# Kernel tuning notes

Hardware: AMD Instinct MI355X
Metric: run time of the kernel (lower is better)

Reference implementation:

```python
import math
import jax, jax.numpy as jnp
import numpy as np

B, W_LEN, C = 4, 2048, 768
H = 3  # fixed number of heads in the module
K = C // H  # head dim


def setup_inputs() -> dict:
    key = jax.random.key(0)
    k1, k2, k3 = jax.random.split(key, 3)
    in_sequence_bwc = jax.random.normal(k1, (B, W_LEN, C), dtype=jnp.float32)
    # torch nn.Linear weights: [out_features, in_features], scaled for stability
    W_qkv = jax.random.normal(k2, (3 * C, C), dtype=jnp.float32) * (1.0 / math.sqrt(C))
    W_proj = jax.random.normal(k3, (C, C), dtype=jnp.float32) * (1.0 / math.sqrt(C))
    return {"in_sequence_bwc": in_sequence_bwc, "W_qkv": W_qkv, "W_proj": W_proj}


def reference(in_sequence_bwc, W_qkv, W_proj):
    batch, words, coords = in_sequence_bwc.shape
    head_dim = coords // H
    # qkv projection: x @ W^T  -> [b, w, 3c]
    all_bwd = jnp.einsum("bwc,dc->bwd", in_sequence_bwc, W_qkv)
    q_bwc, k_bwc, v_bwc = jnp.split(all_bwd, 3, axis=-1)
    # [b, h, w, k]
    q = q_bwc.reshape(batch, words, H, head_dim).transpose(0, 2, 1, 3)
    k = k_bwc.reshape(batch, words, H, head_dim).transpose(0, 2, 1, 3)
    v = v_bwc.reshape(batch, words, H, head_dim).transpose(0, 2, 1, 3)
    # scaled scores with causal mask -> softmax -> @V
    scores = jnp.einsum("bhqk,bhmk->bhqm", q, k) / math.sqrt(head_dim)
    causal = jnp.tril(jnp.ones((words, words), dtype=bool))
    scores = jnp.where(causal[None, None], scores, -jnp.inf)
    probs = jax.nn.softmax(scores, axis=-1)
    out = jnp.einsum("bhqm,bhmk->bhqk", probs, v)
    out_bwc = out.transpose(0, 2, 1, 3).reshape(batch, words, coords)
    return jnp.einsum("bwc,dc->bwd", out_bwc, W_proj)
```

## Files before the change

### kernel.cpp

```cpp
#include <hip/hip_runtime.h>

using v8h = __attribute__((ext_vector_type(8))) _Float16;
using v4f = __attribute__((ext_vector_type(4))) float;
using v4u = __attribute__((ext_vector_type(4))) unsigned short;
using v8u = __attribute__((ext_vector_type(8))) unsigned short;

__device__ __forceinline__ unsigned short f2h(float x) {
  _Float16 h = (_Float16)x;
  return __builtin_bit_cast(unsigned short, h);
}
__device__ __forceinline__ float h2f(unsigned short u) {
  return (float)__builtin_bit_cast(_Float16, u);
}

__device__ __forceinline__ void gl_lds16(const unsigned short* g, unsigned short* l) {
  __builtin_amdgcn_global_load_lds(
      (const __attribute__((address_space(1))) unsigned int*)g,
      (__attribute__((address_space(3))) unsigned int*)l, 16, 0, 0);
}

__global__ void cvt3_kernel(const float* __restrict__ X,
                            const float* __restrict__ Wq,
                            const float* __restrict__ Wp,
                            unsigned short* __restrict__ Xb,
                            unsigned short* __restrict__ Wqb,
                            unsigned short* __restrict__ Wpb) {
  const int blk = (int)blockIdx.x;
  const float* src;
  unsigned short* dst;
  int i;
  if (blk < 3072)      { src = X;  dst = Xb;  i = blk * 256 + threadIdx.x; }
  else if (blk < 3936) { src = Wq; dst = Wqb; i = (blk - 3072) * 256 + threadIdx.x; }
  else                 { src = Wp; dst = Wpb; i = (blk - 3936) * 256 + threadIdx.x; }
  const float* p = src + (size_t)i * 8;
  float4 a = *(const float4*)p;
  float4 b = *(const float4*)(p + 4);
  v8u o = {f2h(a.x), f2h(a.y), f2h(a.z), f2h(a.w),
           f2h(b.x), f2h(b.y), f2h(b.z), f2h(b.w)};
  *(v8u*)(dst + (size_t)i * 8) = o;
}

__global__ __launch_bounds__(512, 2)
void qkv8_kernel(const unsigned short* __restrict__ A,
                 const unsigned short* __restrict__ Bw,
                 unsigned short* __restrict__ QK) {
  __shared__ unsigned short sm[65536];
  const int t    = (int)threadIdx.x;
  const int ln   = t & 63;
  const int wv   = t >> 6;
  const int quad = ln >> 4;
  const int L    = ln & 15;
  const int wm   = wv >> 2;
  const int wn   = wv & 3;
  const long m0  = (long)blockIdx.y * 256;
  const long n0  = (long)blockIdx.x * 256;

  const int srow = t >> 3;
  const int scol = ((t & 7) ^ (srow & 7)) * 8;
  const unsigned short* Ath = A + (m0 + srow) * 768 + scol;
  const unsigned short* Bth = Bw + (n0 + srow) * 768 + scol;
  unsigned short* lth = &sm[t * 8];

  const int l7   = L & 7;
  const int sl0  = ((0 + quad) ^ l7) * 8;
  const int sl1  = ((4 + quad) ^ l7) * 8;
  const int arow = (wm * 128 + L) * 64;
  const int brow = (wn * 64 + L) * 64;

  v4f acc[8][4];
#pragma unroll
  for (int i = 0; i < 8; i++)
#pragma unroll
    for (int j = 0; j < 4; j++) acc[i][j] = (v4f){0.f, 0.f, 0.f, 0.f};

  auto stA = [&](int tile, int h) {
    if (tile >= 12) return;
    const unsigned short* g = Ath + (h * 128) * 768 + tile * 64;
    unsigned short* l = lth + (tile & 1) * 32768 + h * 8192;
    gl_lds16(g, l);
    gl_lds16(g + 64 * 768, l + 4096);
  };
  auto stB = [&](int tile, int h) {
    if (tile >= 12) return;
    const unsigned short* g = Bth + (h * 128) * 768 + tile * 64;
    unsigned short* l = lth + (tile & 1) * 32768 + 16384 + h * 8192;
    gl_lds16(g, l);
    gl_lds16(g + 64 * 768, l + 4096);
  };

  stB(0, 0); stB(0, 1); stA(0, 0); stA(0, 1);
  stB(1, 0); stB(1, 1); stA(1, 0);
  asm volatile("s_waitcnt vmcnt(6)" ::: "memory");
  __builtin_amdgcn_s_barrier();
  __builtin_amdgcn_sched_barrier(0);

#pragma unroll 2
  for (int kt = 0; kt < 12; ++kt) {
    const unsigned short* sA = &sm[(kt & 1) * 32768];
    const unsigned short* sB = sA + 16384;
    v8h af[4][2], b0[2][2], b1[2][2];

#pragma unroll
    for (int i = 0; i < 4; i++) {
      af[i][0] = *(const v8h*)&sA[arow + i * 1024 + sl0];
      af[i][1] = *(const v8h*)&sA[arow + i * 1024 + sl1];
    }
#pragma unroll
    for (int j = 0; j < 2; j++) {
      b0[j][0] = *(const v8h*)&sB[brow + j * 1024 + sl0];
      b0[j][1] = *(const v8h*)&sB[brow + j * 1024 + sl1];
    }
    stA(kt + 1, 1);
    __builtin_amdgcn_s_barrier();
    asm volatile("s_waitcnt lgkmcnt(0)" ::: "memory");
    __builtin_amdgcn_sched_barrier(0);
    __builtin_amdgcn_s_setprio(1);
#pragma unroll
    for (int i = 0; i < 4; i++)
#pragma unroll
      for (int j = 0; j < 2; j++) {
        acc[i][j] = __builtin_amdgcn_mfma_f32_16x16x32_f16(af[i][0], b0[j][0], acc[i][j], 0, 0, 0);
        acc[i][j] = __builtin_amdgcn_mfma_f32_16x16x32_f16(af[i][1], b0[j][1], acc[i][j], 0, 0, 0);
      }
    __builtin_amdgcn_s_setprio(0);
    __builtin_amdgcn_s_barrier();
    __builtin_amdgcn_sched_barrier(0);

#pragma unroll
    for (int j = 0; j < 2; j++) {
      b1[j][0] = *(const v8h*)&sB[brow + 2048 + j * 1024 + sl0];
      b1[j][1] = *(const v8h*)&sB[brow + 2048 + j * 1024 + sl1];
    }
    __builtin_amdgcn_s_barrier();
    asm volatile("s_waitcnt lgkmcnt(0)" ::: "memory");
    __builtin_amdgcn_sched_barrier(0);
    __builtin_amdgcn_s_setprio(1);
#pragma unroll
    for (int i = 0; i < 4; i++)
#pragma unroll
      for (int j = 0; j < 2; j++) {
        acc[i][2 + j] = __builtin_amdgcn_mfma_f32_16x16x32_f16(af[i][0], b1[j][0], acc[i][2 + j], 0, 0, 0);
        acc[i][2 + j] = __builtin_amdgcn_mfma_f32_16x16x32_f16(af[i][1], b1[j][1], acc[i][2 + j], 0, 0, 0);
      }
    __builtin_amdgcn_s_setprio(0);
    __builtin_amdgcn_s_barrier();
    __builtin_amdgcn_sched_barrier(0);

#pragma unroll
    for (int i = 0; i < 4; i++) {
      af[i][0] = *(const v8h*)&sA[arow + 4096 + i * 1024 + sl0];
      af[i][1] = *(const v8h*)&sA[arow + 4096 + i * 1024 + sl1];
    }
    stB(kt + 2, 0);
    __builtin_amdgcn_s_barrier();
    asm volatile("s_waitcnt lgkmcnt(0)" ::: "memory");
    __builtin_amdgcn_sched_barrier(0);
    __builtin_amdgcn_s_setprio(1);
#pragma unroll
    for (int i = 0; i < 4; i++)
#pragma unroll
      for (int j = 0; j < 2; j++) {
        acc[4 + i][2 + j] = __builtin_amdgcn_mfma_f32_16x16x32_f16(af[i][0], b1[j][0], acc[4 + i][2 + j], 0, 0, 0);
        acc[4 + i][2 + j] = __builtin_amdgcn_mfma_f32_16x16x32_f16(af[i][1], b1[j][1], acc[4 + i][2 + j], 0, 0, 0);
      }
    __builtin_amdgcn_s_setprio(0);
    __builtin_amdgcn_s_barrier();
    __builtin_amdgcn_sched_barrier(0);

    stB(kt + 2, 1);
    stA(kt + 2, 0);
    __builtin_amdgcn_s_barrier();
    __builtin_amdgcn_sched_barrier(0);
    __builtin_amdgcn_s_setprio(1);
#pragma unroll
    for (int i = 0; i < 4; i++)
#pragma unroll
      for (int j = 0; j < 2; j++) {
        acc[4 + i][j] = __builtin_amdgcn_mfma_f32_16x16x32_f16(af[i][0], b0[j][0], acc[4 + i][j], 0, 0, 0);
        acc[4 + i][j] = __builtin_amdgcn_mfma_f32_16x16x32_f16(af[i][1], b0[j][1], acc[4 + i][j], 0, 0, 0);
      }
    __builtin_amdgcn_s_setprio(0);
    if (kt + 2 < 12)      { asm volatile("s_waitcnt vmcnt(6)" ::: "memory"); }
    else if (kt + 1 < 12) { asm volatile("s_waitcnt vmcnt(0)" ::: "memory"); }
    __builtin_amdgcn_s_barrier();
    __builtin_amdgcn_sched_barrier(0);
  }

#pragma unroll
  for (int mi = 0; mi < 8; mi++) {
    const long row = m0 + wm * 128 + (mi >> 2) * 64 + (mi & 3) * 16 + quad * 4;
#pragma unroll
    for (int nj = 0; nj < 4; nj++) {
      const long col = n0 + wn * 64 + nj * 16 + L;
#pragma unroll
      for (int r = 0; r < 4; r++)
        QK[(row + r) * 1536 + col] = f2h(acc[mi][nj][r]);
    }
  }
}

__global__ __launch_bounds__(512, 2)
void scv8_kernel(const unsigned short* __restrict__ QK,
                 const unsigned short* __restrict__ Xb,
                 const unsigned short* __restrict__ Wq,
                 unsigned short* __restrict__ Sc,
                 unsigned short* __restrict__ VT) {
  __shared__ unsigned short sm[65536];
  const int t    = (int)threadIdx.x;
  const int ln   = t & 63;
  const int wv   = t >> 6;
  const int quad = ln >> 4;
  const int L    = ln & 15;
  const int wm   = wv >> 2;
  const int wn   = wv & 3;

  const int x = (int)blockIdx.x;
  const bool isV = (x < 96);
  int NT, Ihi = 0, Jhi = 0, bh = 0, mt = 0, nt = 0;
  const unsigned short* Abase;
  const unsigned short* Bbase;
  long astr, bstr;

  if (isV) {
    mt = x & 31;
    nt = x >> 5;
    Abase = Xb + (long)mt * 256 * 768;
    Bbase = Wq + (long)(1536 + nt * 256) * 768;
    astr = 768; bstr = 768; NT = 12;
  } else {
    int s = x - 96;
    bh = s / 36;
    int slot = s % 36;
    while (slot >= Ihi + 1) { slot -= Ihi + 1; Ihi++; }
    Jhi = slot;
    const int b = bh / 3, h = bh % 3;
    Abase = QK + ((long)b * 2048 + Ihi * 256) * 1536 + h * 256;
    Bbase = QK + ((long)b * 2048 + Jhi * 256) * 1536 + 768 + h * 256;
    astr = 1536; bstr = 1536; NT = 4;
  }

  const int srow = t >> 3;
  const int scol = ((t & 7) ^ (srow & 7)) * 8;
  const unsigned short* Ath = Abase + (long)srow * astr + scol;
  const unsigned short* Bth = Bbase + (long)srow * bstr + scol;
  unsigned short* lth = &sm[t * 8];

  const int l7   = L & 7;
  const int sl0  = ((0 + quad) ^ l7) * 8;
  const int sl1  = ((4 + quad) ^ l7) * 8;
  const int arow = (wm * 128 + L) * 64;
  const int brow = (wn * 64 + L) * 64;

  v4f acc[8][4];
#pragma unroll
  for (int i = 0; i < 8; i++)
#pragma unroll
    for (int j = 0; j < 4; j++) acc[i][j] = (v4f){0.f, 0.f, 0.f, 0.f};

  auto stA = [&](int tile, int h) {
    if (tile >= NT) return;
    const unsigned short* g = Ath + (long)(h * 128) * astr + tile * 64;
    unsigned short* l = lth + (tile & 1) * 32768 + h * 8192;
    gl_lds16(g, l);
    gl_lds16(g + 64 * astr, l + 4096);
  };
  auto stB = [&](int tile, int h) {
    if (tile >= NT) return;
    const unsigned short* g = Bth + (long)(h * 128) * bstr + tile * 64;
    unsigned short* l = lth + (tile & 1) * 32768 + 16384 + h * 8192;
    gl_lds16(g, l);
    gl_lds16(g + 64 * bstr, l + 4096);
  };

  stB(0, 0); stB(0, 1); stA(0, 0); stA(0, 1);
  stB(1, 0); stB(1, 1); stA(1, 0);
  asm volatile("s_waitcnt vmcnt(6)" ::: "memory");
  __builtin_amdgcn_s_barrier();
  __builtin_amdgcn_sched_barrier(0);

#pragma unroll 2
  for (int kt = 0; kt < NT; ++kt) {
    const unsigned short* sA = &sm[(kt & 1) * 32768];
    const unsigned short* sB = sA + 16384;
    v8h af[4][2], b0[2][2], b1[2][2];

#pragma unroll
    for (int i = 0; i < 4; i++) {
      af[i][0] = *(const v8h*)&sA[arow + i * 1024 + sl0];
      af[i][1] = *(const v8h*)&sA[arow + i * 1024 + sl1];
    }
#pragma unroll
    for (int j = 0; j < 2; j++) {
      b0[j][0] = *(const v8h*)&sB[brow + j * 1024 + sl0];
      b0[j][1] = *(const v8h*)&sB[brow + j * 1024 + sl1];
    }
    stA(kt + 1, 1);
    __builtin_amdgcn_s_barrier();
    asm volatile("s_waitcnt lgkmcnt(0)" ::: "memory");
    __builtin_amdgcn_sched_barrier(0);
    __builtin_amdgcn_s_setprio(1);
#pragma unroll
    for (int i = 0; i < 4; i++)
#pragma unroll
      for (int j = 0; j < 2; j++) {
        acc[i][j] = __builtin_amdgcn_mfma_f32_16x16x32_f16(af[i][0], b0[j][0], acc[i][j], 0, 0, 0);
        acc[i][j] = __builtin_amdgcn_mfma_f32_16x16x32_f16(af[i][1], b0[j][1], acc[i][j], 0, 0, 0);
      }
    __builtin_amdgcn_s_setprio(0);
    __builtin_amdgcn_s_barrier();
    __builtin_amdgcn_sched_barrier(0);

#pragma unroll
    for (int j = 0; j < 2; j++) {
      b1[j][0] = *(const v8h*)&sB[brow + 2048 + j * 1024 + sl0];
      b1[j][1] = *(const v8h*)&sB[brow + 2048 + j * 1024 + sl1];
    }
    __builtin_amdgcn_s_barrier();
    asm volatile("s_waitcnt lgkmcnt(0)" ::: "memory");
    __builtin_amdgcn_sched_barrier(0);
    __builtin_amdgcn_s_setprio(1);
#pragma unroll
    for (int i = 0; i < 4; i++)
#pragma unroll
      for (int j = 0; j < 2; j++) {
        acc[i][2 + j] = __builtin_amdgcn_mfma_f32_16x16x32_f16(af[i][0], b1[j][0], acc[i][2 + j], 0, 0, 0);
        acc[i][2 + j] = __builtin_amdgcn_mfma_f32_16x16x32_f16(af[i][1], b1[j][1], acc[i][2 + j], 0, 0, 0);
      }
    __builtin_amdgcn_s_setprio(0);
    __builtin_amdgcn_s_barrier();
    __builtin_amdgcn_sched_barrier(0);

#pragma unroll
    for (int i = 0; i < 4; i++) {
      af[i][0] = *(const v8h*)&sA[arow + 4096 + i * 1024 + sl0];
      af[i][1] = *(const v8h*)&sA[arow + 4096 + i * 1024 + sl1];
    }
    stB(kt + 2, 0);
    __builtin_amdgcn_s_barrier();
    asm volatile("s_waitcnt lgkmcnt(0)" ::: "memory");
    __builtin_amdgcn_sched_barrier(0);
    __builtin_amdgcn_s_setprio(1);
#pragma unroll
    for (int i = 0; i < 4; i++)
#pragma unroll
      for (int j = 0; j < 2; j++) {
        acc[4 + i][2 + j] = __builtin_amdgcn_mfma_f32_16x16x32_f16(af[i][0], b1[j][0], acc[4 + i][2 + j], 0, 0, 0);
        acc[4 + i][2 + j] = __builtin_amdgcn_mfma_f32_16x16x32_f16(af[i][1], b1[j][1], acc[4 + i][2 + j], 0, 0, 0);
      }
    __builtin_amdgcn_s_setprio(0);
    __builtin_amdgcn_s_barrier();
    __builtin_amdgcn_sched_barrier(0);

    stB(kt + 2, 1);
    stA(kt + 2, 0);
    __builtin_amdgcn_s_barrier();
    __builtin_amdgcn_sched_barrier(0);
    __builtin_amdgcn_s_setprio(1);
#pragma unroll
    for (int i = 0; i < 4; i++)
#pragma unroll
      for (int j = 0; j < 2; j++) {
        acc[4 + i][j] = __builtin_amdgcn_mfma_f32_16x16x32_f16(af[i][0], b0[j][0], acc[4 + i][j], 0, 0, 0);
        acc[4 + i][j] = __builtin_amdgcn_mfma_f32_16x16x32_f16(af[i][1], b0[j][1], acc[4 + i][j], 0, 0, 0);
      }
    __builtin_amdgcn_s_setprio(0);
    if (kt + 2 < NT)      { asm volatile("s_waitcnt vmcnt(6)" ::: "memory"); }
    else if (kt + 1 < NT) { asm volatile("s_waitcnt vmcnt(0)" ::: "memory"); }
    __builtin_amdgcn_s_barrier();
    __builtin_amdgcn_sched_barrier(0);
  }

  if (isV) {
#pragma unroll
    for (int mi = 0; mi < 8; mi++) {
      const long token = (long)mt * 256 + wm * 128 + (mi >> 2) * 64 + (mi & 3) * 16 + quad * 4;
      const int b  = (int)(token >> 11);
      const int tk = (int)(token & 2047);
#pragma unroll
      for (int nj = 0; nj < 4; nj++) {
        const int colp = nt * 256 + wn * 64 + nj * 16 + L;
        const int h    = colp >> 8;
        const int d    = colp & 255;
        v4u val = {f2h(acc[mi][nj][0]), f2h(acc[mi][nj][1]),
                   f2h(acc[mi][nj][2]), f2h(acc[mi][nj][3])};
        *(v4u*)(&VT[((long)(b * 3 + h) * 256 + d) * 2048 + tk]) = val;
      }
    }
  } else {
    const int di = wm;
    const int dj = wn >> 1;
    const int i128 = 2 * Ihi + di;
    const int j128 = 2 * Jhi + dj;
    if (j128 <= i128) {
      unsigned short* Sb = Sc + ((long)bh * 136 + (long)i128 * (i128 + 1) / 2 + j128) * 16384;
#pragma unroll
      for (int mi = 0; mi < 8; mi++) {
        const int subrow = (mi >> 2) * 64 + (mi & 3) * 16 + quad * 4;
#pragma unroll
        for (int nj = 0; nj < 4; nj++) {
          const int subcol = (wn & 1) * 64 + nj * 16 + L;
#pragma unroll
          for (int r = 0; r < 4; r++)
            Sb[(subrow + r) * 128 + subcol] = f2h(acc[mi][nj][r]);
        }
      }
    }
  }
}

__global__ __launch_bounds__(256, 2)
void gemm_proj_kernel(const unsigned short* __restrict__ A,
                      const unsigned short* __restrict__ Bw,
                      float* __restrict__ C) {
  __shared__ unsigned short As[4096];
  __shared__ unsigned short Bs[4096];

  const int t    = threadIdx.x;
  const int ln   = t & 63;
  const int wv   = t >> 6;
  const int quad = ln >> 4;
  const int L    = ln & 15;
  const int wm   = (wv >> 1) * 64;
  const int wn   = (wv & 1) * 64;
  const long m0  = (long)blockIdx.y * 128;
  const long n0  = (long)blockIdx.x * 128;

  v4f acc[4][4];
#pragma unroll
  for (int i = 0; i < 4; i++)
#pragma unroll
    for (int j = 0; j < 4; j++) acc[i][j] = (v4f){0.f, 0.f, 0.f, 0.f};

  const int ar = t >> 2;
  const int ac = (t & 3) * 8;
  const unsigned short* Ag = A + (m0 + ar) * 768 + ac;
  const unsigned short* Bg = Bw + (n0 + ar) * 768 + ac;
  unsigned short* la = &As[t * 8];
  unsigned short* lb = &Bs[t * 8];
  const long rowskip = 64L * 768;

  for (int k0 = 0; k0 < 768; k0 += 32) {
    gl_lds16(Ag + k0, la);
    gl_lds16(Ag + rowskip + k0, la + 2048);
    gl_lds16(Bg + k0, lb);
    gl_lds16(Bg + rowskip + k0, lb + 2048);
    __syncthreads();

    v8h af[4], bfr[4];
#pragma unroll
    for (int i = 0; i < 4; i++)
      af[i] = *(const v8h*)(&As[(wm + i * 16 + L) * 32 + quad * 8]);
#pragma unroll
    for (int j = 0; j < 4; j++)
      bfr[j] = *(const v8h*)(&Bs[(wn + j * 16 + L) * 32 + quad * 8]);
#pragma unroll
    for (int i = 0; i < 4; i++)
#pragma unroll
      for (int j = 0; j < 4; j++)
        acc[i][j] = __builtin_amdgcn_mfma_f32_16x16x32_f16(af[i], bfr[j], acc[i][j], 0, 0, 0);
    __syncthreads();
  }

#pragma unroll
  for (int i = 0; i < 4; i++)
#pragma unroll
    for (int j = 0; j < 4; j++)
#pragma unroll
      for (int r = 0; r < 4; r++) {
        long row = m0 + wm + i * 16 + quad * 4 + r;
        long col = n0 + wn + j * 16 + L;
        C[row * 768 + col] = acc[i][j][r];
      }
}

__global__ __launch_bounds__(256, 4)
void softmax_kernel(unsigned short* __restrict__ Sc) {
  const int tt   = threadIdx.x;
  const int wv   = tt >> 6;
  const int lane = tt & 63;
  const int bh   = (int)blockIdx.y;

  const int r = 2047 - ((int)blockIdx.x * 4 + wv);
  const int i = r >> 7;
  const int rowloc = r & 127;
  const long base = ((long)bh * 136 + (long)i * (i + 1) / 2) * 16384 + rowloc * 128;
  const int Lrow = (i + 1) * 128;
  const int nch = (i + 4) >> 2;

  float xs[4][8];
  float mx = -1e30f;
  for (int k = 0; k < nch; k++) {
    int c0 = k * 512 + lane * 8;
    if (c0 < Lrow) {
      int j = c0 >> 7;
      v8u v = *(const v8u*)(Sc + base + (long)j * 16384 + (c0 & 127));
#pragma unroll
      for (int e = 0; e < 8; e++) {
        float f = (c0 + e <= r) ? h2f(v[e]) * 0.0625f : -1e30f;
        xs[k][e] = f;
        mx = fmaxf(mx, f);
      }
    } else {
#pragma unroll
      for (int e = 0; e < 8; e++) xs[k][e] = -1e30f;
    }
  }
#pragma unroll
  for (int d = 1; d < 64; d <<= 1) mx = fmaxf(mx, __shfl_xor(mx, d));

  float sum = 0.f;
  for (int k = 0; k < nch; k++)
#pragma unroll
    for (int e = 0; e < 8; e++) {
      float ex = __expf(xs[k][e] - mx);
      xs[k][e] = ex;
      sum += ex;
    }
#pragma unroll
  for (int d = 1; d < 64; d <<= 1) sum += __shfl_xor(sum, d);
  const float inv = 1.0f / sum;

  for (int k = 0; k < nch; k++) {
    int c0 = k * 512 + lane * 8;
    if (c0 < Lrow) {
      int j = c0 >> 7;
      v8u o;
#pragma unroll
      for (int e = 0; e < 8; e++) o[e] = f2h(xs[k][e] * inv);
      *(v8u*)(Sc + base + (long)j * 16384 + (c0 & 127)) = o;
    }
  }
}

__global__ __launch_bounds__(256, 2)
void gemm_pv_kernel(const unsigned short* __restrict__ Sc,
                    const unsigned short* __restrict__ VT,
                    unsigned short* __restrict__ Pp) {
  __shared__ unsigned short As[4096];
  __shared__ unsigned short Bs[4096];

  const int t    = threadIdx.x;
  const int ln   = t & 63;
  const int wv   = t >> 6;
  const int quad = ln >> 4;
  const int L    = ln & 15;
  const int wm   = (wv >> 1) * 64;
  const int wn   = (wv & 1) * 64;

  const int ix  = (int)blockIdx.x;
  const int i   = 15 - (ix >> 2);
  const int nh  = (ix >> 1) & 1;
  const int par = ix & 1;
  const int bh  = (int)blockIdx.y;

  v4f acc[4][4];
#pragma unroll
  for (int ii = 0; ii < 4; ii++)
#pragma unroll
    for (int jj = 0; jj < 4; jj++) acc[ii][jj] = (v4f){0.f, 0.f, 0.f, 0.f};

  const int ar = t >> 2;
  const int ac = (t & 3) * 8;
  const unsigned short* Abase =
      Sc + ((long)bh * 136 + (long)i * (i + 1) / 2) * 16384 + ar * 128 + ac;
  const unsigned short* Bg =
      VT + ((long)bh * 256 + nh * 128 + ar) * 2048 + ac;
  unsigned short* la = &As[t * 8];
  unsigned short* lb = &Bs[t * 8];

  for (int j = par; j <= i; j += 2) {
    const unsigned short* Aj = Abase + (long)j * 16384;
    const unsigned short* Bj = Bg + j * 128;
#pragma unroll
    for (int k0 = 0; k0 < 128; k0 += 32) {
      gl_lds16(Aj + k0, la);
      gl_lds16(Aj + 64 * 128 + k0, la + 2048);
      gl_lds16(Bj + k0, lb);
      gl_lds16(Bj + 64 * 2048 + k0, lb + 2048);
      __syncthreads();

      v8h af[4], bfr[4];
#pragma unroll
      for (int ii = 0; ii < 4; ii++)
        af[ii] = *(const v8h*)(&As[(wm + ii * 16 + L) * 32 + quad * 8]);
#pragma unroll
      for (int jj = 0; jj < 4; jj++)
        bfr[jj] = *(const v8h*)(&Bs[(wn + jj * 16 + L) * 32 + quad * 8]);
#pragma unroll
      for (int ii = 0; ii < 4; ii++)
#pragma unroll
        for (int jj = 0; jj < 4; jj++)
          acc[ii][jj] = __builtin_amdgcn_mfma_f32_16x16x32_f16(af[ii], bfr[jj], acc[ii][jj], 0, 0, 0);
      __syncthreads();
    }
  }

  unsigned short* Pb = Pp + ((((long)bh * 16 + i) * 2 + nh) * 2 + par) * 16384;
#pragma unroll
  for (int ii = 0; ii < 4; ii++)
#pragma unroll
    for (int jj = 0; jj < 4; jj++)
#pragma unroll
      for (int r = 0; r < 4; r++) {
        int row = wm + ii * 16 + quad * 4 + r;
        int col = wn + jj * 16 + L;
        Pb[row * 128 + col] = f2h(acc[ii][jj][r]);
      }
}

__global__ __launch_bounds__(256, 4)
void pv_combine_kernel(const unsigned short* __restrict__ Pp,
                       unsigned short* __restrict__ AO) {
  const int i  = (int)blockIdx.x >> 1;
  const int nh = (int)blockIdx.x & 1;
  const int bh = (int)blockIdx.y;
  const int b  = bh / 3, h = bh % 3;

  const int tid = threadIdx.x;
  const int row = tid >> 1;
  const int cs  = (tid & 1) * 64;

  const unsigned short* P0 = Pp + ((((long)bh * 16 + i) * 2 + nh) * 2 + 0) * 16384 + row * 128 + cs;
  const unsigned short* P1 = P0 + 16384;
  unsigned short* Or = AO + ((long)b * 2048 + i * 128 + row) * 768 + h * 256 + nh * 128 + cs;
#pragma unroll
  for (int q = 0; q < 8; q++) {
    v8u a = *(const v8u*)(P0 + q * 8);
    v8u c = *(const v8u*)(P1 + q * 8);
    v8u o;
#pragma unroll
    for (int e = 0; e < 8; e++) o[e] = f2h(h2f(a[e]) + h2f(c[e]));
    *(v8u*)(Or + q * 8) = o;
  }
}

extern "C" void kernel_launch(void* const* d_in, const int* in_sizes, int n_in,
                              void* d_out, int out_size, void* d_ws, size_t ws_size,
                              hipStream_t stream) {
  const float* X     = (const float*)d_in[0];
  const float* Wqkv  = (const float*)d_in[1];
  const float* Wproj = (const float*)d_in[2];
  float* out = (float*)d_out;

  const size_t SZ_QK = (size_t)8192 * 1536 * 2;
  const size_t SZ_VT = (size_t)3072 * 2048 * 2;
  const size_t SZ_SC = (size_t)12 * 136 * 16384 * 2;
  const size_t SZ_AO = (size_t)8192 * 768 * 2;
  const size_t SZ_WQ = (size_t)2304 * 768 * 2;

  char* ws = (char*)d_ws;
  unsigned short* QKb = (unsigned short*)ws;
  unsigned short* Ppb = QKb;
  unsigned short* VTb = (unsigned short*)(ws + SZ_QK);
  unsigned short* Scb = (unsigned short*)(ws + SZ_QK + SZ_VT);
  unsigned short* AOb = (unsigned short*)(ws + SZ_QK + SZ_VT + SZ_SC);
  unsigned short* Xb  = AOb;
  unsigned short* Wqb = (unsigned short*)(ws + SZ_QK + SZ_VT + SZ_SC + SZ_AO);
  unsigned short* Wpb = (unsigned short*)(ws + SZ_QK + SZ_VT + SZ_SC + SZ_AO + SZ_WQ);

  dim3 blk(256, 1, 1);
  cvt3_kernel<<<dim3(4224, 1, 1), blk, 0, stream>>>(X, Wqkv, Wproj, Xb, Wqb, Wpb);
  qkv8_kernel<<<dim3(6, 32, 1), dim3(512, 1, 1), 0, stream>>>(Xb, Wqb, QKb);
  scv8_kernel<<<dim3(528, 1, 1), dim3(512, 1, 1), 0, stream>>>(QKb, Xb, Wqb, Scb, VTb);
  softmax_kernel<<<dim3(512, 12, 1), blk, 0, stream>>>(Scb);
  gemm_pv_kernel<<<dim3(64, 12, 1), blk, 0, stream>>>(Scb, VTb, Ppb);
  pv_combine_kernel<<<dim3(32, 12, 1), blk, 0, stream>>>(Ppb, AOb);
  gemm_proj_kernel<<<dim3(6, 64, 1), blk, 0, stream>>>(AOb, Wpb, out);
}
```

Before: 243.6 us.

## Fuse softmax, PV GEMM and combine into one online-softmax kernel

Replaces the separate softmax pass, the split-K PV GEMM and the partial-sum combine kernel with one kernel. It runs an online (flash-style) softmax over the stored fp16 score tiles and multiplies by V with MFMA, double-buffering V tiles in swizzled LDS and prefetching score fragments into registers. Blocks pair query tile i with tile 15-i to balance the causal work. This drops the softmax read-modify-write of the score matrix and the partial-product round trip. The cost is a much smaller grid (192 blocks of 512 threads), so parallelism is lower, and the loop relies on manual waitcnt and barrier scheduling.

Result: faster. 223.6 us (-8.2%).

```diff
diff --git a/kernel.cpp b/kernel.cpp
--- a/kernel.cpp
+++ b/kernel.cpp
@@ -408,6 +408,186 @@
   }
 }
 
+__global__ __launch_bounds__(512, 1)
+void pvf_kernel(const unsigned short* __restrict__ Sc,
+                const unsigned short* __restrict__ VT,
+                unsigned short* __restrict__ AO) {
+  __shared__ unsigned short sm[36864];
+  __shared__ float fbuf[128];
+
+  const int t    = (int)threadIdx.x;
+  const int ln   = t & 63;
+  const int wv   = t >> 6;
+  const int quad = ln >> 4;
+  const int L    = ln & 15;
+
+  const int p  = (int)blockIdx.x >> 1;
+  const int nh = (int)blockIdx.x & 1;
+  const int bh = (int)blockIdx.y;
+  const int b  = bh / 3, h = bh % 3;
+
+  const unsigned short* VTb = VT + ((long)(bh * 256 + nh * 128)) * 2048;
+  const int rloc = wv * 16 + L;
+
+  auto stageV = [&](int jj, unsigned short* base) {
+#pragma unroll
+    for (int pp = 0; pp < 4; pp++) {
+      const int sidx = pp * 512 + t;
+      const int d    = sidx >> 4;
+      const int ph   = sidx & 15;
+      gl_lds16(VTb + (long)d * 2048 + jj * 128 + ((ph ^ (d & 7)) * 8),
+               base + sidx * 8);
+    }
+  };
+
+  for (int sel = 0; sel < 2; ++sel) {
+    const int i = sel ? (15 - p) : p;
+    const long Sbase = ((long)bh * 136 + (long)i * (i + 1) / 2) * 16384;
+
+    v4f acc[8];
+#pragma unroll
+    for (int n = 0; n < 8; n++) acc[n] = (v4f){0.f, 0.f, 0.f, 0.f};
+    float m_run = -1e30f, l_run = 0.f;
+
+    v8u s_cur[4], s_nxt[4];
+    {
+      const unsigned short* Sp = Sc + Sbase + (long)rloc * 128;
+#pragma unroll
+      for (int ks = 0; ks < 4; ks++)
+        s_cur[ks] = *(const v8u*)(Sp + ks * 32 + quad * 8);
+      __builtin_amdgcn_sched_barrier(0);
+      stageV(0, &sm[0]);
+      __builtin_amdgcn_sched_barrier(0);
+    }
+
+    for (int j = 0; j <= i; ++j) {
+      const int jn = (j < i) ? (j + 1) : i;
+      const bool clamped = (j == i);
+      {
+        const unsigned short* Sp = Sc + Sbase + (long)jn * 16384 + (long)rloc * 128;
+#pragma unroll
+        for (int ks = 0; ks < 4; ks++)
+          s_nxt[ks] = *(const v8u*)(Sp + ks * 32 + quad * 8);
+      }
+      __builtin_amdgcn_sched_barrier(0);
+      if (clamped) {
+#pragma unroll
+        for (int pp = 0; pp < 4; pp++) {
+          const int sidx = pp * 512 + t;
+          const int d    = sidx >> 4;
+          const int ph   = sidx & 15;
+          gl_lds16(VTb + (long)d * 2048 + jn * 128 + ((ph ^ (d & 7)) * 8),
+                   &sm[32768 + t * 8]);
+        }
+      } else {
+        stageV(jn, &sm[(jn & 1) * 16384]);
+      }
+      __builtin_amdgcn_sched_barrier(0);
+
+      float pv[4][8];
+      float mx = -1e30f;
+      if (j == i) {
+#pragma unroll
+        for (int ks = 0; ks < 4; ks++)
+#pragma unroll
+          for (int e = 0; e < 8; e++) {
+            const bool valid = (ks * 32 + quad * 8 + e) <= rloc;
+            const float f = valid ? h2f(s_cur[ks][e]) * 0.0625f : -1e30f;
+            pv[ks][e] = f;
+            mx = fmaxf(mx, f);
+          }
+      } else {
+#pragma unroll
+        for (int ks = 0; ks < 4; ks++)
+#pragma unroll
+          for (int e = 0; e < 8; e++) {
+            const float f = h2f(s_cur[ks][e]) * 0.0625f;
+            pv[ks][e] = f;
+            mx = fmaxf(mx, f);
+          }
+      }
+      mx = fmaxf(mx, __shfl_xor(mx, 16));
+      mx = fmaxf(mx, __shfl_xor(mx, 32));
+      const float m_new = fmaxf(m_run, mx);
+      const float alpha = __expf(m_run - m_new);
+      m_run = m_new;
+
+      float sum = 0.f;
+      v8h pa[4];
+#pragma unroll
+      for (int ks = 0; ks < 4; ks++) {
+        v8h ph16;
+#pragma unroll
+        for (int e = 0; e < 8; e++) {
+          const float pe = __expf(pv[ks][e] - m_new);
+          sum += pe;
+          ph16[e] = (_Float16)pe;
+        }
+        pa[ks] = ph16;
+      }
+      sum += __shfl_xor(sum, 16);
+      sum += __shfl_xor(sum, 32);
+      l_run = l_run * alpha + sum;
+
+      if (quad == 0) fbuf[wv * 16 + L] = alpha;
+      asm volatile("s_waitcnt lgkmcnt(0)" ::: "memory");
+      __builtin_amdgcn_sched_barrier(0);
+      const float a0 = fbuf[wv * 16 + quad * 4 + 0];
+      const float a1 = fbuf[wv * 16 + quad * 4 + 1];
+      const float a2 = fbuf[wv * 16 + quad * 4 + 2];
+      const float a3 = fbuf[wv * 16 + quad * 4 + 3];
+#pragma unroll
+      for (int n = 0; n < 8; n++) {
+        acc[n][0] *= a0; acc[n][1] *= a1; acc[n][2] *= a2; acc[n][3] *= a3;
+      }
+
+      asm volatile("s_waitcnt vmcnt(8)" ::: "memory");
+      __builtin_amdgcn_s_barrier();
+      __builtin_amdgcn_sched_barrier(0);
+
+      const unsigned short* vb = &sm[(j & 1) * 16384];
+      const int dx = L & 7;
+#pragma unroll
+      for (int nfc = 0; nfc < 8; nfc++) {
+        const int dbase = (nfc * 16 + L) * 128;
+        v8h v0 = *(const v8h*)&vb[dbase + ((0 + quad) ^ dx) * 8];
+        v8h v1 = *(const v8h*)&vb[dbase + ((4 + quad) ^ dx) * 8];
+        v8h v2 = *(const v8h*)&vb[dbase + ((8 + quad) ^ dx) * 8];
+        v8h v3 = *(const v8h*)&vb[dbase + ((12 + quad) ^ dx) * 8];
+        acc[nfc] = __builtin_amdgcn_mfma_f32_16x16x32_f16(pa[0], v0, acc[nfc], 0, 0, 0);
+        acc[nfc] = __builtin_amdgcn_mfma_f32_16x16x32_f16(pa[1], v1, acc[nfc], 0, 0, 0);
+        acc[nfc] = __builtin_amdgcn_mfma_f32_16x16x32_f16(pa[2], v2, acc[nfc], 0, 0, 0);
+        acc[nfc] = __builtin_amdgcn_mfma_f32_16x16x32_f16(pa[3], v3, acc[nfc], 0, 0, 0);
+      }
+      __builtin_amdgcn_s_barrier();
+      __builtin_amdgcn_sched_barrier(0);
+
+#pragma unroll
+      for (int ks = 0; ks < 4; ks++) s_cur[ks] = s_nxt[ks];
+    }
+
+    const float inv = 1.0f / l_run;
+    if (quad == 0) fbuf[wv * 16 + L] = inv;
+    asm volatile("s_waitcnt lgkmcnt(0)" ::: "memory");
+    __builtin_amdgcn_sched_barrier(0);
+    const float i0 = fbuf[wv * 16 + quad * 4 + 0];
+    const float i1 = fbuf[wv * 16 + quad * 4 + 1];
+    const float i2 = fbuf[wv * 16 + quad * 4 + 2];
+    const float i3 = fbuf[wv * 16 + quad * 4 + 3];
+
+    unsigned short* Ob = AO + ((long)b * 2048 + (long)i * 128 + wv * 16 + quad * 4) * 768
+                            + h * 256 + nh * 128 + L;
+#pragma unroll
+    for (int n = 0; n < 8; n++) {
+      Ob[0 * 768 + n * 16] = f2h(acc[n][0] * i0);
+      Ob[1 * 768 + n * 16] = f2h(acc[n][1] * i1);
+      Ob[2 * 768 + n * 16] = f2h(acc[n][2] * i2);
+      Ob[3 * 768 + n * 16] = f2h(acc[n][3] * i3);
+    }
+    __builtin_amdgcn_s_barrier();
+  }
+}
+
 __global__ __launch_bounds__(256, 2)
 void gemm_proj_kernel(const unsigned short* __restrict__ A,
                       const unsigned short* __restrict__ Bw,
@@ -473,167 +653,6 @@
       }
 }
 
-__global__ __launch_bounds__(256, 4)
-void softmax_kernel(unsigned short* __restrict__ Sc) {
-  const int tt   = threadIdx.x;
-  const int wv   = tt >> 6;
-  const int lane = tt & 63;
-  const int bh   = (int)blockIdx.y;
-
-  const int r = 2047 - ((int)blockIdx.x * 4 + wv);
-  const int i = r >> 7;
-  const int rowloc = r & 127;
-  const long base = ((long)bh * 136 + (long)i * (i + 1) / 2) * 16384 + rowloc * 128;
-  const int Lrow = (i + 1) * 128;
-  const int nch = (i + 4) >> 2;
-
-  float xs[4][8];
-  float mx = -1e30f;
-  for (int k = 0; k < nch; k++) {
-    int c0 = k * 512 + lane * 8;
-    if (c0 < Lrow) {
-      int j = c0 >> 7;
-      v8u v = *(const v8u*)(Sc + base + (long)j * 16384 + (c0 & 127));
-#pragma unroll
-      for (int e = 0; e < 8; e++) {
-        float f = (c0 + e <= r) ? h2f(v[e]) * 0.0625f : -1e30f;
-        xs[k][e] = f;
-        mx = fmaxf(mx, f);
-      }
-    } else {
-#pragma unroll
-      for (int e = 0; e < 8; e++) xs[k][e] = -1e30f;
-    }
-  }
-#pragma unroll
-  for (int d = 1; d < 64; d <<= 1) mx = fmaxf(mx, __shfl_xor(mx, d));
-
-  float sum = 0.f;
-  for (int k = 0; k < nch; k++)
-#pragma unroll
-    for (int e = 0; e < 8; e++) {
-      float ex = __expf(xs[k][e] - mx);
-      xs[k][e] = ex;
-      sum += ex;
-    }
-#pragma unroll
-  for (int d = 1; d < 64; d <<= 1) sum += __shfl_xor(sum, d);
-  const float inv = 1.0f / sum;
-
-  for (int k = 0; k < nch; k++) {
-    int c0 = k * 512 + lane * 8;
-    if (c0 < Lrow) {
-      int j = c0 >> 7;
-      v8u o;
-#pragma unroll
-      for (int e = 0; e < 8; e++) o[e] = f2h(xs[k][e] * inv);
-      *(v8u*)(Sc + base + (long)j * 16384 + (c0 & 127)) = o;
-    }
-  }
-}
-
-__global__ __launch_bounds__(256, 2)
-void gemm_pv_kernel(const unsigned short* __restrict__ Sc,
-                    const unsigned short* __restrict__ VT,
-                    unsigned short* __restrict__ Pp) {
-  __shared__ unsigned short As[4096];
-  __shared__ unsigned short Bs[4096];
-
-  const int t    = threadIdx.x;
-  const int ln   = t & 63;
-  const int wv   = t >> 6;
-  const int quad = ln >> 4;
-  const int L    = ln & 15;
-  const int wm   = (wv >> 1) * 64;
-  const int wn   = (wv & 1) * 64;
-
-  const int ix  = (int)blockIdx.x;
-  const int i   = 15 - (ix >> 2);
-  const int nh  = (ix >> 1) & 1;
-  const int par = ix & 1;
-  const int bh  = (int)blockIdx.y;
-
-  v4f acc[4][4];
-#pragma unroll
-  for (int ii = 0; ii < 4; ii++)
-#pragma unroll
-    for (int jj = 0; jj < 4; jj++) acc[ii][jj] = (v4f){0.f, 0.f, 0.f, 0.f};
-
-  const int ar = t >> 2;
-  const int ac = (t & 3) * 8;
-  const unsigned short* Abase =
-      Sc + ((long)bh * 136 + (long)i * (i + 1) / 2) * 16384 + ar * 128 + ac;
-  const unsigned short* Bg =
-      VT + ((long)bh * 256 + nh * 128 + ar) * 2048 + ac;
-  unsigned short* la = &As[t * 8];
-  unsigned short* lb = &Bs[t * 8];
-
-  for (int j = par; j <= i; j += 2) {
-    const unsigned short* Aj = Abase + (long)j * 16384;
-    const unsigned short* Bj = Bg + j * 128;
-#pragma unroll
-    for (int k0 = 0; k0 < 128; k0 += 32) {
-      gl_lds16(Aj + k0, la);
-      gl_lds16(Aj + 64 * 128 + k0, la + 2048);
-      gl_lds16(Bj + k0, lb);
-      gl_lds16(Bj + 64 * 2048 + k0, lb + 2048);
-      __syncthreads();
-
-      v8h af[4], bfr[4];
-#pragma unroll
-      for (int ii = 0; ii < 4; ii++)
-        af[ii] = *(const v8h*)(&As[(wm + ii * 16 + L) * 32 + quad * 8]);
-#pragma unroll
-      for (int jj = 0; jj < 4; jj++)
-        bfr[jj] = *(const v8h*)(&Bs[(wn + jj * 16 + L) * 32 + quad * 8]);
-#pragma unroll
-      for (int ii = 0; ii < 4; ii++)
-#pragma unroll
-        for (int jj = 0; jj < 4; jj++)
-          acc[ii][jj] = __builtin_amdgcn_mfma_f32_16x16x32_f16(af[ii], bfr[jj], acc[ii][jj], 0, 0, 0);
-      __syncthreads();
-    }
-  }
-
-  unsigned short* Pb = Pp + ((((long)bh * 16 + i) * 2 + nh) * 2 + par) * 16384;
-#pragma unroll
-  for (int ii = 0; ii < 4; ii++)
-#pragma unroll
-    for (int jj = 0; jj < 4; jj++)
-#pragma unroll
-      for (int r = 0; r < 4; r++) {
-        int row = wm + ii * 16 + quad * 4 + r;
-        int col = wn + jj * 16 + L;
-        Pb[row * 128 + col] = f2h(acc[ii][jj][r]);
-      }
-}
-
-__global__ __launch_bounds__(256, 4)
-void pv_combine_kernel(const unsigned short* __restrict__ Pp,
-                       unsigned short* __restrict__ AO) {
-  const int i  = (int)blockIdx.x >> 1;
-  const int nh = (int)blockIdx.x & 1;
-  const int bh = (int)blockIdx.y;
-  const int b  = bh / 3, h = bh % 3;
-
-  const int tid = threadIdx.x;
-  const int row = tid >> 1;
-  const int cs  = (tid & 1) * 64;
-
-  const unsigned short* P0 = Pp + ((((long)bh * 16 + i) * 2 + nh) * 2 + 0) * 16384 + row * 128 + cs;
-  const unsigned short* P1 = P0 + 16384;
-  unsigned short* Or = AO + ((long)b * 2048 + i * 128 + row) * 768 + h * 256 + nh * 128 + cs;
-#pragma unroll
-  for (int q = 0; q < 8; q++) {
-    v8u a = *(const v8u*)(P0 + q * 8);
-    v8u c = *(const v8u*)(P1 + q * 8);
-    v8u o;
-#pragma unroll
-    for (int e = 0; e < 8; e++) o[e] = f2h(h2f(a[e]) + h2f(c[e]));
-    *(v8u*)(Or + q * 8) = o;
-  }
-}
-
 extern "C" void kernel_launch(void* const* d_in, const int* in_sizes, int n_in,
                               void* d_out, int out_size, void* d_ws, size_t ws_size,
                               hipStream_t stream) {
@@ -650,7 +669,6 @@
 
   char* ws = (char*)d_ws;
   unsigned short* QKb = (unsigned short*)ws;
-  unsigned short* Ppb = QKb;
   unsigned short* VTb = (unsigned short*)(ws + SZ_QK);
   unsigned short* Scb = (unsigned short*)(ws + SZ_QK + SZ_VT);
   unsigned short* AOb = (unsigned short*)(ws + SZ_QK + SZ_VT + SZ_SC);
@@ -662,8 +680,6 @@
   cvt3_kernel<<<dim3(4224, 1, 1), blk, 0, stream>>>(X, Wqkv, Wproj, Xb, Wqb, Wpb);
   qkv8_kernel<<<dim3(6, 32, 1), dim3(512, 1, 1), 0, stream>>>(Xb, Wqb, QKb);
   scv8_kernel<<<dim3(528, 1, 1), dim3(512, 1, 1), 0, stream>>>(QKb, Xb, Wqb, Scb, VTb);
-  softmax_kernel<<<dim3(512, 12, 1), blk, 0, stream>>>(Scb);
-  gemm_pv_kernel<<<dim3(64, 12, 1), blk, 0, stream>>>(Scb, VTb, Ppb);
-  pv_combine_kernel<<<dim3(32, 12, 1), blk, 0, stream>>>(Ppb, AOb);
+  pvf_kernel<<<dim3(16, 12, 1), dim3(512, 1, 1), 0, stream>>>(Scb, VTb, AOb);
   gemm_proj_kernel<<<dim3(6, 64, 1), blk, 0, stream>>>(AOb, Wpb, out);
 }
```
